# Kernel optimization log

Hardware: AMD Instinct MI355X
Metric: run time of the kernel (lower is better)

Reference implementation:

```python
import jax, jax.numpy as jnp
import numpy as np

P = 6
CUTOFF = 1.0
N_BASIS = 8
AVG_NEIGH = 16.0
NUM_LAYERS = 2
N, E, MUL, H, F = 8192, 131072, 16, 256, 16


def envelope(d):
    # polynomial cutoff u(x) with p=6 (NequIP/Allegro style)
    x = d / CUTOFF
    p = float(P)
    u = (1.0 - (p + 1.0) * (p + 2.0) / 2.0 * x ** P
         + p * (p + 2.0) * x ** (P + 1)
         - p * (p + 1.0) / 2.0 * x ** (P + 2))
    return jnp.where(x < 1.0, u, 0.0)


def bessel(d):
    k = jnp.arange(1, N_BASIS + 1, dtype=d.dtype)
    return jnp.sqrt(2.0 / CUTOFF) * jnp.sin(k[None, :] * jnp.pi * d[:, None] / CUTOFF) / d[:, None]


def sph_harm(u):
    # real spherical harmonics, ell=0..3, component normalization -> [E,16]
    x, y, z = u[:, 0], u[:, 1], u[:, 2]
    s3 = 3.0 ** 0.5
    s5 = 5.0 ** 0.5
    s15 = 15.0 ** 0.5
    s7 = 7.0 ** 0.5
    c33 = (35.0 / 8.0) ** 0.5
    c32 = 105.0 ** 0.5
    c31 = (21.0 / 8.0) ** 0.5
    one = jnp.ones_like(x)
    comps = [
        one,
        s3 * x, s3 * y, s3 * z,
        s15 * x * y, s15 * y * z, 0.5 * s5 * (3.0 * z * z - 1.0), s15 * x * z, 0.5 * s15 * (x * x - y * y),
        c33 * y * (3.0 * x * x - y * y), c32 * x * y * z, c31 * y * (5.0 * z * z - 1.0),
        0.5 * s7 * (5.0 * z ** 3 - 3.0 * z), c31 * x * (5.0 * z * z - 1.0),
        0.5 * c32 * z * (x * x - y * y), c33 * x * (x * x - 3.0 * y * y),
    ]
    return jnp.stack(comps, axis=1)


def setup_inputs() -> dict:
    key = jax.random.key(0)
    ks = jax.random.split(key, 16)
    dirs = jax.random.normal(ks[0], (E, 3), dtype=jnp.float32)
    dirs = dirs / jnp.linalg.norm(dirs, axis=1, keepdims=True)
    r = jax.random.uniform(ks[1], (E, 1), minval=0.05, maxval=0.95, dtype=jnp.float32)
    vectors = dirs * r
    node_attrs = 0.5 * jax.random.normal(ks[2], (N, F), dtype=jnp.float32)
    senders = jax.random.randint(ks[3], (E,), 0, N, dtype=jnp.int32)
    receivers = jax.random.randint(ks[4], (E,), 0, N, dtype=jnp.int32)

    def gl(k, shape):
        fan_in = shape[-2] if len(shape) >= 2 else 1
        return jax.random.normal(k, shape, dtype=jnp.float32) / jnp.sqrt(float(fan_in))

    return {
        'node_attrs': node_attrs, 'vectors': vectors,
        'senders': senders, 'receivers': receivers,
        'W_e0': gl(ks[5], (N_BASIS + 2 * F, H)), 'b_e0': jnp.zeros((H,), jnp.float32),
        'W_e1': gl(ks[6], (H, H)), 'b_e1': jnp.zeros((H,), jnp.float32),
        'W_v0': gl(ks[7], (H, MUL)),
        'W_lw': gl(ks[8], (NUM_LAYERS, H, MUL)),
        'W_lsh': gl(ks[9], (NUM_LAYERS, 16, 16)),
        'W_ly1': gl(ks[10], (NUM_LAYERS, H + MUL, H)), 'b_ly1': jnp.zeros((NUM_LAYERS, H), jnp.float32),
        'W_ly2': gl(ks[11], (NUM_LAYERS, H, H)), 'b_ly2': jnp.zeros((NUM_LAYERS, H), jnp.float32),
        'W_out': gl(ks[12], (H, 1)),
    }


def reference(node_attrs, vectors, senders, receivers, W_e0, b_e0, W_e1, b_e1, W_v0,
              W_lw, W_lsh, W_ly1, b_ly1, W_ly2, b_ly2, W_out):
    n_nodes = node_attrs.shape[0]
    inv = 1.0 / jnp.sqrt(AVG_NEIGH)
    d = jnp.linalg.norm(vectors, axis=1)                      # [E]
    u = envelope(d)                                           # [E]
    # edge embedding: radial basis + gathered endpoint attrs
    x = jnp.concatenate([bessel(d), node_attrs[senders], node_attrs[receivers]], axis=1)
    x = jax.nn.silu(x @ W_e0 + b_e0)
    x = jax.nn.silu(x @ W_e1 + b_e1)
    x = u[:, None] * x                                        # [E,H]
    Y = sph_harm(vectors / d[:, None])                        # [E,16]
    V = (x @ W_v0)[:, :, None] * Y[:, None, :]                # [E,MUL,16]
    for l in range(NUM_LAYERS):
        w = x @ W_lw[l]                                       # [E,MUL]
        wY = jax.ops.segment_sum(w[:, :, None] * Y[:, None, :], senders, num_segments=n_nodes) * inv
        wY = wY[senders]                                      # [E,MUL,16] gather back
        VV = wY * V                                           # per-edge equivariant product
        V = jnp.einsum('emi,ij->emj', VV, W_lsh[l])
        h = jnp.concatenate([x, VV[:, :, 0]], axis=1)         # scalar (l=0) channel feedback
        y = jax.nn.silu(h @ W_ly1[l] + b_ly1[l])
        y = jax.nn.silu(y @ W_ly2[l] + b_ly2[l])
        x = (x + u[:, None] * y) / jnp.sqrt(2.0)
    edge_out = (x @ W_out) * u[:, None]                       # [E,1]
    node_out = jax.ops.segment_sum(edge_out, receivers, num_segments=n_nodes) * inv
    return node_out                                           # [N,1]
```

## Files before the change

kernel.cpp:

```cpp
#include <hip/hip_runtime.h>
#include <hip/hip_bf16.h>
#include <math.h>

#define H 256
#define F 16
#define MUL 16
#define NB 8
#define LROW 296
#define YROW 264

typedef short bf16x8 __attribute__((ext_vector_type(8)));
typedef short bf16x4 __attribute__((ext_vector_type(4)));
typedef float f32x4 __attribute__((ext_vector_type(4)));
#define MFMA_B16(a, b, c) __builtin_amdgcn_mfma_f32_16x16x32_bf16(a, b, c, 0, 0, 0)

__device__ __forceinline__ float bf2f(__hip_bfloat16 x) { return __bfloat162float(x); }
__device__ __forceinline__ float silu(float x)
{
    return x * __builtin_amdgcn_rcpf(1.f + __expf(-x));
}
__device__ __forceinline__ short f2bs(float x)
{
    __hip_bfloat16 h = __float2bfloat16(x);
    short s; __builtin_memcpy(&s, &h, 2); return s;
}
__device__ __forceinline__ float bs2f(short s)
{
    __hip_bfloat16 h; __builtin_memcpy(&h, &s, 2); return __bfloat162float(h);
}

__global__ __launch_bounds__(256) void k_sniff(const void* vec, int* flag,
                                               int* cnt, int N)
{
    __shared__ int bad;
    int tid = threadIdx.x;
    if (tid == 0) bad = 0;
    __syncthreads();
    const __hip_bfloat16* hp = (const __hip_bfloat16*)vec;
    for (int i = tid; i < 1024; i += 256) {
        float f = bf2f(hp[i]);
        if (!(isfinite(f) && fabsf(f) <= 1.0f)) bad = 1;
    }
    for (int i = tid; i < N; i += 256) cnt[i] = 0;
    __syncthreads();
    if (tid == 0) *flag = bad;
}

struct ConvArgs {
    const void* src[14];
    float* dst[14];
    int cum[15];
};
__global__ __launch_bounds__(256) void k_conv_all(ConvArgs a, const int* __restrict__ flag,
                                                  const int* __restrict__ snd,
                                                  int* __restrict__ cnt, int E)
{
    int gid = blockIdx.x * 256 + threadIdx.x;
    if (gid < E) atomicAdd(&cnt[snd[gid]], 1);
    if (gid >= a.cum[14]) return;
    int k = 0;
    while (gid >= a.cum[k + 1]) k++;
    int i = gid - a.cum[k];
    float v = (*flag) ? ((const float*)a.src[k])[i]
                      : bf2f(((const __hip_bfloat16*)a.src[k])[i]);
    a.dst[k][i] = v;
}

struct SwzArgs {
    const float* src[9];
    __hip_bfloat16* dst[9];
    int K[9], Nc[9], cum[10];
};
__global__ __launch_bounds__(256) void k_swz_all(SwzArgs a)
{
    int gid = blockIdx.x * 256 + threadIdx.x;
    if (gid >= a.cum[9]) return;
    int j = 0;
    while (gid >= a.cum[j + 1]) j++;
    int idx = gid - a.cum[j];
    int kk = idx & 31;
    int n = (idx >> 5) % a.Nc[j];
    int kt = idx / (32 * a.Nc[j]);
    int k = kt * 32 + kk;
    float v = (k < a.K[j]) ? a.src[j][(size_t)k * a.Nc[j] + n] : 0.f;
    a.dst[j][idx] = __float2bfloat16(v);
}

__global__ __launch_bounds__(256) void k_swz_wout(const float* __restrict__ Wout,
                                                  __hip_bfloat16* __restrict__ dst)
{
    int idx = blockIdx.x * 256 + threadIdx.x;
    if (idx >= 8 * 16 * 32) return;
    int kk = idx & 31;
    int n = (idx >> 5) & 15;
    int kt = idx >> 9;
    float v = (n == 0) ? Wout[kt * 32 + kk] : 0.f;
    dst[idx] = __float2bfloat16(v);
}

__global__ __launch_bounds__(256) void k_scan(const int* __restrict__ cnt,
                                              int* __restrict__ off,
                                              int* __restrict__ cur, int N)
{
    __shared__ int sums[256];
    int tid = threadIdx.x;
    int chunk = (N + 255) / 256;
    int base = tid * chunk;
    int s = 0;
    for (int i = 0; i < chunk; i++) { int idx = base + i; if (idx < N) s += cnt[idx]; }
    sums[tid] = s;
    __syncthreads();
    for (int d = 1; d < 256; d <<= 1) {
        int v = (tid >= d) ? sums[tid - d] : 0;
        __syncthreads();
        sums[tid] += v;
        __syncthreads();
    }
    int run = (tid == 0) ? 0 : sums[tid - 1];
    for (int i = 0; i < chunk; i++) {
        int idx = base + i;
        if (idx < N) { off[idx] = run; cur[idx] = run; run += cnt[idx]; }
    }
    if (tid == 255) off[N] = run;
}

__global__ __launch_bounds__(256) void k_cscatter(const int* __restrict__ snd,
                                                  int* __restrict__ cur,
                                                  int* __restrict__ eidx, int E)
{
    int e = blockIdx.x * 256 + threadIdx.x;
    if (e >= E) return;
    int p = atomicAdd(&cur[snd[e]], 1);
    eidx[p] = e;
}


__global__ __launch_bounds__(512, 4) void k_embed_mfma(
    const float* __restrict__ vec, const float* __restrict__ na,
    const int* __restrict__ snd, const int* __restrict__ rcv,
    const __hip_bfloat16* __restrict__ We0s, const float* __restrict__ be0,
    const __hip_bfloat16* __restrict__ We1s, const float* __restrict__ be1,
    const __hip_bfloat16* __restrict__ Wv0s, const __hip_bfloat16* __restrict__ Wlws0,
    float* __restrict__ ubuf, float* __restrict__ Ybuf,
    __hip_bfloat16* __restrict__ xb, float* __restrict__ abuf,
    float* __restrict__ wbuf)
{
    __shared__ __align__(16) __hip_bfloat16 As[64 * LROW];
    __shared__ __align__(16) __hip_bfloat16 Ys[64 * YROW];
    __shared__ float us[64];
    int tid = threadIdx.x;
    int w = tid >> 6, l = tid & 63;
    int lm = l & 15, lq = l >> 4;
    int eb = blockIdx.x * 64;

    bf16x8 w0p[2][2];
#pragma unroll
    for (int kt = 0; kt < 2; kt++)
#pragma unroll
        for (int nt = 0; nt < 2; nt++)
            w0p[kt][nt] = *(const bf16x8*)(We0s + ((size_t)(kt * 256 + w * 32 + nt * 16 + lm) * 32 + lq * 8));

    {
        int el = tid & 63;
        int part = tid >> 6;
        int ge = eb + el;
        const float SQ2 = 1.41421356237309515f;
        const float PI = 3.14159265358979323846f;
        if (part == 0) {
            float vx = vec[3 * ge + 0], vy = vec[3 * ge + 1], vz = vec[3 * ge + 2];
            float d = sqrtf(vx * vx + vy * vy + vz * vz);
            float d3 = d * d * d;
            float d6 = d3 * d3, d7 = d6 * d, d8 = d7 * d;
            float u = 1.f - 28.f * d6 + 48.f * d7 - 21.f * d8;
            u = (d < 1.f) ? u : 0.f;
            ubuf[ge] = u;
            us[el] = u;
            float invd = __builtin_amdgcn_rcpf(d);
#pragma unroll
            for (int k = 1; k <= 4; k++)
                As[el * LROW + (k - 1)] = __float2bfloat16(SQ2 * __sinf((float)k * PI * d) * invd);
        } else if (part == 4) {
            float vx = vec[3 * ge + 0], vy = vec[3 * ge + 1], vz = vec[3 * ge + 2];
            float d = sqrtf(vx * vx + vy * vy + vz * vz);
            float invd = __builtin_amdgcn_rcpf(d);
#pragma unroll
            for (int k = 5; k <= 8; k++)
                As[el * LROW + (k - 1)] = __float2bfloat16(SQ2 * __sinf((float)k * PI * d) * invd);
        } else if (part == 5) {
#pragma unroll
            for (int j = 40; j < 64; j++) As[el * LROW + j] = __float2bfloat16(0.f);
        } else if (part == 1) {
            int s = snd[ge];
#pragma unroll
            for (int j = 0; j < 16; j++)
                As[el * LROW + 8 + j] = __float2bfloat16(na[(size_t)s * F + j]);
        } else if (part == 2) {
            int r = rcv[ge];
#pragma unroll
            for (int j = 0; j < 16; j++)
                As[el * LROW + 24 + j] = __float2bfloat16(na[(size_t)r * F + j]);
        } else if (part == 3) {
            float vx = vec[3 * ge + 0], vy = vec[3 * ge + 1], vz = vec[3 * ge + 2];
            float d = sqrtf(vx * vx + vy * vy + vz * vz);
            float invd = __builtin_amdgcn_rcpf(d);
            float x = vx * invd, y = vy * invd, z = vz * invd;
            const float s3 = 1.7320508075688772f;
            const float s5 = 2.2360679774997896f;
            const float s15 = 3.8729833462074170f;
            const float s7 = 2.6457513110645907f;
            const float c33 = 2.0916500663351889f;
            const float c32 = 10.246950765959598f;
            const float c31 = 1.6201851746019651f;
            float* Yp = Ybuf + (size_t)ge * 16;
            Yp[0] = 1.f;
            Yp[1] = s3 * x;  Yp[2] = s3 * y;  Yp[3] = s3 * z;
            Yp[4] = s15 * x * y;  Yp[5] = s15 * y * z;
            Yp[6] = 0.5f * s5 * (3.f * z * z - 1.f);
            Yp[7] = s15 * x * z;
            Yp[8] = 0.5f * s15 * (x * x - y * y);
            Yp[9] = c33 * y * (3.f * x * x - y * y);
            Yp[10] = c32 * x * y * z;
            Yp[11] = c31 * y * (5.f * z * z - 1.f);
            Yp[12] = 0.5f * s7 * (5.f * z * z * z - 3.f * z);
            Yp[13] = c31 * x * (5.f * z * z - 1.f);
            Yp[14] = 0.5f * c32 * z * (x * x - y * y);
            Yp[15] = c33 * x * (x * x - 3.f * y * y);
        }
    }
    __syncthreads();

    f32x4 acc[4][2];
#pragma unroll
    for (int mt = 0; mt < 4; mt++)
#pragma unroll
        for (int nt = 0; nt < 2; nt++) acc[mt][nt] = (f32x4){0.f, 0.f, 0.f, 0.f};
#pragma unroll
    for (int kt = 0; kt < 2; kt++) {
#pragma unroll
        for (int mt = 0; mt < 4; mt++) {
            bf16x8 bx = *(const bf16x8*)(As + (mt * 16 + lm) * LROW + kt * 32 + lq * 8);
#pragma unroll
            for (int nt = 0; nt < 2; nt++) acc[mt][nt] = MFMA_B16(w0p[kt][nt], bx, acc[mt][nt]);
        }
    }
    bf16x8 w1p[2][2];
#pragma unroll
    for (int kt = 0; kt < 2; kt++)
#pragma unroll
        for (int nt = 0; nt < 2; nt++)
            w1p[kt][nt] = *(const bf16x8*)(We1s + ((size_t)(kt * 256 + w * 32 + nt * 16 + lm) * 32 + lq * 8));
#pragma unroll
    for (int nt = 0; nt < 2; nt++) {
        int cb = w * 32 + nt * 16 + lq * 4;
        f32x4 bb = *(const f32x4*)(be0 + cb);
#pragma unroll
        for (int mt = 0; mt < 4; mt++) {
            int row = mt * 16 + lm;
            bf16x4 v = {f2bs(silu(acc[mt][nt][0] + bb[0])), f2bs(silu(acc[mt][nt][1] + bb[1])),
                        f2bs(silu(acc[mt][nt][2] + bb[2])), f2bs(silu(acc[mt][nt][3] + bb[3]))};
            *(bf16x4*)(Ys + row * YROW + cb) = v;
        }
    }
    __syncthreads();

#pragma unroll
    for (int mt = 0; mt < 4; mt++)
#pragma unroll
        for (int nt = 0; nt < 2; nt++) acc[mt][nt] = (f32x4){0.f, 0.f, 0.f, 0.f};
#pragma unroll
    for (int kt = 0; kt < 8; kt++) {
        bf16x8 aw[2];
#pragma unroll
        for (int nt = 0; nt < 2; nt++)
            aw[nt] = (kt < 2) ? w1p[kt][nt]
                   : *(const bf16x8*)(We1s + ((size_t)(kt * 256 + w * 32 + nt * 16 + lm) * 32 + lq * 8));
#pragma unroll
        for (int mt = 0; mt < 4; mt++) {
            bf16x8 bx = *(const bf16x8*)(Ys + (mt * 16 + lm) * YROW + kt * 32 + lq * 8);
#pragma unroll
            for (int nt = 0; nt < 2; nt++) acc[mt][nt] = MFMA_B16(aw[nt], bx, acc[mt][nt]);
        }
    }
    const __hip_bfloat16* tw = (w < 4) ? Wv0s : Wlws0;
    bf16x8 twp[2];
#pragma unroll
    for (int kt = 0; kt < 2; kt++)
        twp[kt] = *(const bf16x8*)(tw + ((size_t)(kt * 16 + lm) * 32 + lq * 8));
#pragma unroll
    for (int nt = 0; nt < 2; nt++) {
        int cb = w * 32 + nt * 16 + lq * 4;
        f32x4 bb = *(const f32x4*)(be1 + cb);
#pragma unroll
        for (int mt = 0; mt < 4; mt++) {
            int row = mt * 16 + lm;
            float uu = us[row];
            bf16x4 v = {f2bs(silu(acc[mt][nt][0] + bb[0]) * uu),
                        f2bs(silu(acc[mt][nt][1] + bb[1]) * uu),
                        f2bs(silu(acc[mt][nt][2] + bb[2]) * uu),
                        f2bs(silu(acc[mt][nt][3] + bb[3]) * uu)};
            *(bf16x4*)(As + row * LROW + cb) = v;
            *(bf16x4*)(xb + (size_t)(eb + row) * H + cb) = v;
        }
    }
    __syncthreads();

    if (w < 4) {
        f32x4 av = (f32x4){0.f, 0.f, 0.f, 0.f};
#pragma unroll
        for (int kt = 0; kt < 8; kt++) {
            bf16x8 bx = *(const bf16x8*)(As + (w * 16 + lm) * LROW + kt * 32 + lq * 8);
            bf16x8 a_v = (kt < 2) ? twp[kt]
                       : *(const bf16x8*)(Wv0s + ((size_t)(kt * 16 + lm) * 32 + lq * 8));
            av = MFMA_B16(a_v, bx, av);
        }
        *(f32x4*)(abuf + (size_t)(eb + w * 16 + lm) * 16 + lq * 4) = av;
    } else {
        int w2 = w - 4;
        f32x4 aw2 = (f32x4){0.f, 0.f, 0.f, 0.f};
#pragma unroll
        for (int kt = 0; kt < 8; kt++) {
            bf16x8 bx = *(const bf16x8*)(As + (w2 * 16 + lm) * LROW + kt * 32 + lq * 8);
            bf16x8 a_w = (kt < 2) ? twp[kt]
                       : *(const bf16x8*)(Wlws0 + ((size_t)(kt * 16 + lm) * 32 + lq * 8));
            aw2 = MFMA_B16(a_w, bx, aw2);
        }
        *(f32x4*)(wbuf + (size_t)(eb + w2 * 16 + lm) * 16 + lq * 4) = aw2;
    }
}

__global__ __launch_bounds__(256) void k_gather0(
    const int* __restrict__ off, const int* __restrict__ eidx,
    const float* __restrict__ wbuf, const float* __restrict__ Ybuf,
    const float* __restrict__ abuf,
    float* __restrict__ wYn0, __hip_bfloat16* __restrict__ vvbuf)
{
    __shared__ float ws[16][17];
    __shared__ float Ysh[16][17];
    __shared__ float w00[16];
    int tid = threadIdx.x;
    int m = tid >> 4, i = tid & 15;
    for (int nn = 0; nn < 4; nn++) {
        int n = blockIdx.x * 4 + nn;
        int beg = off[n], end = off[n + 1];
        float acc = 0.f;
        for (int c = beg; c < end; c += 16) {
            int ne = min(16, end - c);
            if (m < ne) {
                int e = eidx[c + m];
                ws[m][i] = wbuf[(size_t)e * 16 + i];
                Ysh[m][i] = Ybuf[(size_t)e * 16 + i];
            }
            __syncthreads();
            for (int j2 = 0; j2 < ne; j2++) acc += ws[j2][m] * Ysh[j2][i];
            __syncthreads();
        }
        wYn0[(size_t)n * 256 + m * 16 + i] = acc * 0.25f;
        if (i == 0) w00[m] = acc * 0.25f;
        __syncthreads();
        float w0i = w00[i];
        for (int c = beg + m; c < end; c += 16) {
            int e = eidx[c];
            float a = abuf[(size_t)e * 16 + i];
            vvbuf[(size_t)e * 16 + i] = __float2bfloat16(w0i * a);
        }
        __syncthreads();
    }
}

__global__ __launch_bounds__(256) void k_gather1(
    const int* __restrict__ off, const int* __restrict__ eidx,
    const float* __restrict__ wbuf, const float* __restrict__ Ybuf,
    const float* __restrict__ abuf,
    const float* __restrict__ wYn0, const float* __restrict__ Wlsh,
    __hip_bfloat16* __restrict__ vvbuf, float* __restrict__ nacc)
{
    __shared__ float ws[16][17];
    __shared__ float Ysh[16][17];
    __shared__ float qsh[16][17];
    __shared__ float w10[16];
    int tid = threadIdx.x;
    int m = tid >> 4, i = tid & 15;
    if (tid < 4) nacc[blockIdx.x * 4 + tid] = 0.f;
    for (int nn = 0; nn < 4; nn++) {
        int n = blockIdx.x * 4 + nn;
        int beg = off[n], end = off[n + 1];
        float acc = 0.f;
        for (int c = beg; c < end; c += 16) {
            int ne = min(16, end - c);
            if (m < ne) {
                int e = eidx[c + m];
                ws[m][i] = wbuf[(size_t)e * 16 + i];
                Ysh[m][i] = Ybuf[(size_t)e * 16 + i];
            }
            __syncthreads();
            for (int j2 = 0; j2 < ne; j2++) acc += ws[j2][m] * Ysh[j2][i];
            __syncthreads();
        }
        if (i == 0) w10[m] = acc * 0.25f;
        qsh[m][i] = wYn0[(size_t)n * 256 + m * 16 + i] * Wlsh[i * 16];
        __syncthreads();
        float w1i = w10[i];
        for (int c = beg + m; c < end; c += 16) {
            int e = eidx[c];
            float a = abuf[(size_t)e * 16 + i];
            float t = 0.f;
#pragma unroll
            for (int j = 0; j < 4; j++) {
                f32x4 yv = *(const f32x4*)(Ybuf + (size_t)e * 16 + 4 * j);
                t += qsh[i][4 * j + 0] * yv[0] + qsh[i][4 * j + 1] * yv[1]
                   + qsh[i][4 * j + 2] * yv[2] + qsh[i][4 * j + 3] * yv[3];
            }
            vvbuf[(size_t)e * 16 + i] = __float2bfloat16(w1i * a * t);
        }
        __syncthreads();
    }
}

__global__ __launch_bounds__(512, 4) void k_layer_mfma(
    __hip_bfloat16* __restrict__ xb, const float* __restrict__ ubuf,
    const __hip_bfloat16* __restrict__ vvbuf, const int* __restrict__ rcv,
    const __hip_bfloat16* __restrict__ W1s, const float* __restrict__ b1,
    const __hip_bfloat16* __restrict__ W2s, const float* __restrict__ b2,
    const __hip_bfloat16* __restrict__ Wlwn, float* __restrict__ wbufn,
    const __hip_bfloat16* __restrict__ Wouts, float* __restrict__ nacc,
    int layer)
{
    __shared__ __align__(16) __hip_bfloat16 As[64 * LROW];
    __shared__ __align__(16) __hip_bfloat16 Ys[64 * YROW];
    int tid = threadIdx.x;
    int w = tid >> 6, l = tid & 63;
    int lm = l & 15, lq = l >> 4;
    int eb = blockIdx.x * 64;

    bf16x8 w1p[2][2];
#pragma unroll
    for (int kt = 0; kt < 2; kt++)
#pragma unroll
        for (int nt = 0; nt < 2; nt++)
            w1p[kt][nt] = *(const bf16x8*)(W1s + ((size_t)(kt * 256 + w * 32 + nt * 16 + lm) * 32 + lq * 8));

#pragma unroll
    for (int i = 0; i < 4; i++) {
        int c = tid + 512 * i;
        int row = c >> 5, kc = c & 31;
        *(bf16x8*)(As + row * LROW + kc * 8) =
            *(const bf16x8*)(xb + (size_t)(eb + row) * H + kc * 8);
    }
    {
        int el = tid & 63;
        int mh = (tid >> 6) * 2;
        int ge = eb + el;
        *(unsigned int*)(As + el * LROW + 256 + mh) =
            *(const unsigned int*)((const short*)vvbuf + (size_t)ge * 16 + mh);
        if (tid < 64) {
#pragma unroll
            for (int j = 0; j < 16; j++) As[tid * LROW + 272 + j] = __float2bfloat16(0.f);
        }
    }
    __syncthreads();

    float uu[4];
#pragma unroll
    for (int mt = 0; mt < 4; mt++) uu[mt] = ubuf[eb + mt * 16 + lm];

    f32x4 acc[4][2];
#pragma unroll
    for (int mt = 0; mt < 4; mt++)
#pragma unroll
        for (int nt = 0; nt < 2; nt++) acc[mt][nt] = (f32x4){0.f, 0.f, 0.f, 0.f};
#pragma unroll
    for (int kt = 0; kt < 9; kt++) {
        bf16x8 aw[2];
#pragma unroll
        for (int nt = 0; nt < 2; nt++)
            aw[nt] = (kt < 2) ? w1p[kt][nt]
                   : *(const bf16x8*)(W1s + ((size_t)(kt * 256 + w * 32 + nt * 16 + lm) * 32 + lq * 8));
#pragma unroll
        for (int mt = 0; mt < 4; mt++) {
            bf16x8 bx = *(const bf16x8*)(As + (mt * 16 + lm) * LROW + kt * 32 + lq * 8);
#pragma unroll
            for (int nt = 0; nt < 2; nt++) acc[mt][nt] = MFMA_B16(aw[nt], bx, acc[mt][nt]);
        }
    }
    bf16x8 w2p[2][2];
#pragma unroll
    for (int kt = 0; kt < 2; kt++)
#pragma unroll
        for (int nt = 0; nt < 2; nt++)
            w2p[kt][nt] = *(const bf16x8*)(W2s + ((size_t)(kt * 256 + w * 32 + nt * 16 + lm) * 32 + lq * 8));
#pragma unroll
    for (int nt = 0; nt < 2; nt++) {
        int cb = w * 32 + nt * 16 + lq * 4;
        f32x4 bb = *(const f32x4*)(b1 + cb);
#pragma unroll
        for (int mt = 0; mt < 4; mt++) {
            int row = mt * 16 + lm;
            bf16x4 v = {f2bs(silu(acc[mt][nt][0] + bb[0])), f2bs(silu(acc[mt][nt][1] + bb[1])),
                        f2bs(silu(acc[mt][nt][2] + bb[2])), f2bs(silu(acc[mt][nt][3] + bb[3]))};
            *(bf16x4*)(Ys + row * YROW + cb) = v;
        }
    }
    __syncthreads();

#pragma unroll
    for (int mt = 0; mt < 4; mt++)
#pragma unroll
        for (int nt = 0; nt < 2; nt++) acc[mt][nt] = (f32x4){0.f, 0.f, 0.f, 0.f};
#pragma unroll
    for (int kt = 0; kt < 8; kt++) {
        bf16x8 aw[2];
#pragma unroll
        for (int nt = 0; nt < 2; nt++)
            aw[nt] = (kt < 2) ? w2p[kt][nt]
                   : *(const bf16x8*)(W2s + ((size_t)(kt * 256 + w * 32 + nt * 16 + lm) * 32 + lq * 8));
#pragma unroll
        for (int mt = 0; mt < 4; mt++) {
            bf16x8 bx = *(const bf16x8*)(Ys + (mt * 16 + lm) * YROW + kt * 32 + lq * 8);
#pragma unroll
            for (int nt = 0; nt < 2; nt++) acc[mt][nt] = MFMA_B16(aw[nt], bx, acc[mt][nt]);
        }
    }
    const __hip_bfloat16* tw = (layer == 0) ? Wlwn : Wouts;
    bf16x8 twp[2];
#pragma unroll
    for (int kt = 0; kt < 2; kt++)
        twp[kt] = *(const bf16x8*)(tw + ((size_t)(kt * 16 + lm) * 32 + lq * 8));
    const float rs2 = 0.70710678118654752f;
#pragma unroll
    for (int nt = 0; nt < 2; nt++) {
        int cb = w * 32 + nt * 16 + lq * 4;
        f32x4 bb = *(const f32x4*)(b2 + cb);
#pragma unroll
        for (int mt = 0; mt < 4; mt++) {
            int row = mt * 16 + lm;
            bf16x4 xo = *(const bf16x4*)(As + row * LROW + cb);
            bf16x4 v;
#pragma unroll
            for (int r = 0; r < 4; r++) {
                float xn = (bs2f(xo[r]) + uu[mt] * silu(acc[mt][nt][r] + bb[r])) * rs2;
                v[r] = f2bs(xn);
            }
            *(bf16x4*)(As + row * LROW + cb) = v;
            if (layer == 0) *(bf16x4*)(xb + (size_t)(eb + row) * H + cb) = v;
        }
    }
    __syncthreads();

    if (layer == 0) {
        if (w < 4) {
            f32x4 cw = (f32x4){0.f, 0.f, 0.f, 0.f};
#pragma unroll
            for (int kt = 0; kt < 8; kt++) {
                bf16x8 bx = *(const bf16x8*)(As + (w * 16 + lm) * LROW + kt * 32 + lq * 8);
                bf16x8 a = (kt < 2) ? twp[kt]
                         : *(const bf16x8*)(Wlwn + ((size_t)(kt * 16 + lm) * 32 + lq * 8));
                cw = MFMA_B16(a, bx, cw);
            }
            *(f32x4*)(wbufn + (size_t)(eb + w * 16 + lm) * 16 + lq * 4) = cw;
        }
    } else {
        if (w < 4) {
            f32x4 co = (f32x4){0.f, 0.f, 0.f, 0.f};
#pragma unroll
            for (int kt = 0; kt < 8; kt++) {
                bf16x8 bx = *(const bf16x8*)(As + (w * 16 + lm) * LROW + kt * 32 + lq * 8);
                bf16x8 a = (kt < 2) ? twp[kt]
                         : *(const bf16x8*)(Wouts + ((size_t)(kt * 16 + lm) * 32 + lq * 8));
                co = MFMA_B16(a, bx, co);
            }
            if (lq == 0) {
                int e = eb + w * 16 + lm;
                atomicAdd(&nacc[rcv[e]], co[0] * ubuf[e]);
            }
        }
    }
}

__global__ __launch_bounds__(256) void k_final(
    const float* __restrict__ nacc, void* __restrict__ out, const int* __restrict__ flag,
    float inv, int N)
{
    int n = blockIdx.x * 256 + threadIdx.x;
    if (n >= N) return;
    float v = nacc[n] * inv;
    if (*flag) ((float*)out)[n] = v;
    else       ((__hip_bfloat16*)out)[n] = __float2bfloat16(v);
}

extern "C" void kernel_launch(void* const* d_in, const int* in_sizes, int n_in,
                              void* d_out, int out_size, void* d_ws, size_t ws_size,
                              hipStream_t stream)
{
    const int E = in_sizes[2];
    const int N = in_sizes[0] / F;
    (void)n_in; (void)ws_size; (void)out_size;

    char* wsb = (char*)d_ws;
    size_t off = 0;
    int* flag = (int*)wsb; off += 256;

    const int fidx[14] = {0, 1, 4, 5, 6, 7, 8, 9, 10, 11, 12, 13, 14, 15};
    float* canon[14];
    for (int k = 0; k < 14; k++) {
        canon[k] = (float*)(wsb + off);
        off += (size_t)in_sizes[fidx[k]] * 4;
        off = (off + 255) & ~(size_t)255;
    }
    const float* naC   = canon[0];
    const float* vecC  = canon[1];
    const float* We0C  = canon[2];
    const float* be0C  = canon[3];
    const float* We1C  = canon[4];
    const float* be1C  = canon[5];
    const float* Wv0C  = canon[6];
    const float* WlwC  = canon[7];
    const float* WlshC = canon[8];
    const float* Wly1C = canon[9];
    const float* bly1C = canon[10];
    const float* Wly2C = canon[11];
    const float* bly2C = canon[12];
    const float* WoutC = canon[13];

    __hip_bfloat16* We0s  = (__hip_bfloat16*)(wsb + off); off += 64 * 256 * 2;
    __hip_bfloat16* We1s  = (__hip_bfloat16*)(wsb + off); off += 256 * 256 * 2;
    __hip_bfloat16* Wv0s  = (__hip_bfloat16*)(wsb + off); off += 256 * 16 * 2;
    __hip_bfloat16* Wlws0 = (__hip_bfloat16*)(wsb + off); off += 256 * 16 * 2;
    __hip_bfloat16* Wlws1 = (__hip_bfloat16*)(wsb + off); off += 256 * 16 * 2;
    __hip_bfloat16* W1s0  = (__hip_bfloat16*)(wsb + off); off += 288 * 256 * 2;
    __hip_bfloat16* W1s1  = (__hip_bfloat16*)(wsb + off); off += 288 * 256 * 2;
    __hip_bfloat16* W2s0  = (__hip_bfloat16*)(wsb + off); off += 256 * 256 * 2;
    __hip_bfloat16* W2s1  = (__hip_bfloat16*)(wsb + off); off += 256 * 256 * 2;
    __hip_bfloat16* Wouts = (__hip_bfloat16*)(wsb + off); off += 256 * 16 * 2;
    off = (off + 255) & ~(size_t)255;

    __hip_bfloat16* xbuf = (__hip_bfloat16*)(wsb + off); off += (size_t)E * H * 2;
    float* wYn0 = (float*)(wsb + off); off += (size_t)N * H * 4;
    __hip_bfloat16* vvbuf = (__hip_bfloat16*)(wsb + off); off += (size_t)E * 16 * 2;
    float* ubuf = (float*)(wsb + off); off += (size_t)E * 4;
    float* Ybuf = (float*)(wsb + off); off += (size_t)E * 16 * 4;
    float* abuf = (float*)(wsb + off); off += (size_t)E * 16 * 4;
    float* wbuf = (float*)(wsb + off); off += (size_t)E * 16 * 4;
    float* nacc = (float*)(wsb + off); off += (size_t)N * 4;
    int* cnt  = (int*)(wsb + off); off += (size_t)N * 4;
    int* offb = (int*)(wsb + off); off += (size_t)(N + 1) * 4;
    int* cur  = (int*)(wsb + off); off += (size_t)N * 4;
    int* eidx = (int*)(wsb + off); off += (size_t)E * 4;

    const int* snd = (const int*)d_in[2];
    const int* rcv = (const int*)d_in[3];
    const float inv = 0.25f;
    const int nb64 = E / 64;

    k_sniff<<<1, 256, 0, stream>>>(d_in[1], flag, cnt, N);
    {
        ConvArgs ca;
        int c = 0;
        for (int k = 0; k < 14; k++) {
            ca.src[k] = d_in[fidx[k]];
            ca.dst[k] = canon[k];
            ca.cum[k] = c;
            c += in_sizes[fidx[k]];
        }
        ca.cum[14] = c;
        k_conv_all<<<(c + 255) / 256, 256, 0, stream>>>(ca, flag, snd, cnt, E);
    }

    {
        SwzArgs sa;
        const float* srcs[9] = {We0C, We1C, Wv0C, WlwC, WlwC + 256 * 16,
                                Wly1C, Wly1C + 272 * 256, Wly2C, Wly2C + 256 * 256};
        __hip_bfloat16* dsts[9] = {We0s, We1s, Wv0s, Wlws0, Wlws1, W1s0, W1s1, W2s0, W2s1};
        int Ks[9]    = {40, 256, 256, 256, 256, 272, 272, 256, 256};
        int Ncs[9]   = {256, 256, 16, 16, 16, 256, 256, 256, 256};
        int Kpads[9] = {64, 256, 256, 256, 256, 288, 288, 256, 256};
        int c = 0;
        for (int j = 0; j < 9; j++) {
            sa.src[j] = srcs[j]; sa.dst[j] = dsts[j];
            sa.K[j] = Ks[j]; sa.Nc[j] = Ncs[j];
            sa.cum[j] = c;
            c += (Kpads[j] >> 5) * Ncs[j] * 32;
        }
        sa.cum[9] = c;
        k_swz_all<<<(c + 255) / 256, 256, 0, stream>>>(sa);
    }
    k_swz_wout<<<16, 256, 0, stream>>>(WoutC, Wouts);

    k_scan<<<1, 256, 0, stream>>>(cnt, offb, cur, N);
    k_cscatter<<<(E + 255) / 256, 256, 0, stream>>>(snd, cur, eidx, E);

    k_embed_mfma<<<nb64, 512, 0, stream>>>(vecC, naC, snd, rcv,
                                           We0s, be0C, We1s, be1C, Wv0s, Wlws0,
                                           ubuf, Ybuf, xbuf, abuf, wbuf);

    k_gather0<<<N / 4, 256, 0, stream>>>(offb, eidx, wbuf, Ybuf, abuf, wYn0, vvbuf);
    k_layer_mfma<<<nb64, 512, 0, stream>>>(xbuf, ubuf, vvbuf, rcv,
                                           W1s0, bly1C, W2s0, bly2C,
                                           Wlws1, wbuf,
                                           (const __hip_bfloat16*)nullptr, (float*)nullptr, 0);
    k_gather1<<<N / 4, 256, 0, stream>>>(offb, eidx, wbuf, Ybuf, abuf, wYn0, WlshC,
                                         vvbuf, nacc);
    k_layer_mfma<<<nb64, 512, 0, stream>>>(xbuf, ubuf, vvbuf, rcv,
                                           W1s1, bly1C + H, W2s1, bly2C + H,
                                           (const __hip_bfloat16*)nullptr, (float*)nullptr,
                                           Wouts, nacc, 1);

    k_final<<<(N + 255) / 256, 256, 0, stream>>>(nacc, d_out, flag, inv, N);
}
```

Measured before the change: 345.5 us.

## Assign one wavefront per node in gather kernels instead of serial node loop

The two per-node gather kernels previously processed their four nodes one after another with the full 256-thread block, syncing twice per 16-edge chunk. Now each 64-lane wavefront owns one node, with per-wave shared-memory slices and four accumulators per lane, so the four nodes proceed concurrently. Iteration count is bounded by the largest degree among the four nodes, so waves with fewer edges sit idle at the block barriers. Shared memory per block grows fourfold.

```diff
diff --git a/kernel.cpp b/kernel.cpp
--- a/kernel.cpp
+++ b/kernel.cpp
@@ -334,36 +334,57 @@
     const float* __restrict__ abuf,
     float* __restrict__ wYn0, __hip_bfloat16* __restrict__ vvbuf)
 {
-    __shared__ float ws[16][17];
-    __shared__ float Ysh[16][17];
-    __shared__ float w00[16];
+    __shared__ float ws[4][16][17];
+    __shared__ float Ysh[4][16][17];
+    __shared__ float w00s[4][16];
     int tid = threadIdx.x;
-    int m = tid >> 4, i = tid & 15;
-    for (int nn = 0; nn < 4; nn++) {
-        int n = blockIdx.x * 4 + nn;
-        int beg = off[n], end = off[n + 1];
-        float acc = 0.f;
-        for (int c = beg; c < end; c += 16) {
-            int ne = min(16, end - c);
-            if (m < ne) {
-                int e = eidx[c + m];
-                ws[m][i] = wbuf[(size_t)e * 16 + i];
-                Ysh[m][i] = Ybuf[(size_t)e * 16 + i];
+    int w = tid >> 6, l = tid & 63;
+    int js = l >> 4, i = l & 15;
+    int n0 = blockIdx.x * 4;
+    int n = n0 + w;
+    int beg = off[n], end = off[n + 1];
+    int o0 = off[n0], o1 = off[n0 + 1], o2 = off[n0 + 2], o3 = off[n0 + 3], o4 = off[n0 + 4];
+    int m01 = max(o1 - o0, o2 - o1), m23 = max(o3 - o2, o4 - o3);
+    int maxc = (max(m01, m23) + 15) >> 4;
+    float acc[4] = {0.f, 0.f, 0.f, 0.f};
+    for (int r = 0; r < maxc; r++) {
+        int c = beg + r * 16;
+        int ne = min(16, end - c);
+        if (ne > 0) {
+#pragma unroll
+            for (int k = 0; k < 4; k++) {
+                int j = js + 4 * k;
+                if (j < ne) {
+                    int e = eidx[c + j];
+                    ws[w][j][i]  = wbuf[(size_t)e * 16 + i];
+                    Ysh[w][j][i] = Ybuf[(size_t)e * 16 + i];
+                }
             }
-            __syncthreads();
-            for (int j2 = 0; j2 < ne; j2++) acc += ws[j2][m] * Ysh[j2][i];
-            __syncthreads();
-        }
-        wYn0[(size_t)n * 256 + m * 16 + i] = acc * 0.25f;
-        if (i == 0) w00[m] = acc * 0.25f;
+        }
         __syncthreads();
-        float w0i = w00[i];
-        for (int c = beg + m; c < end; c += 16) {
-            int e = eidx[c];
-            float a = abuf[(size_t)e * 16 + i];
-            vvbuf[(size_t)e * 16 + i] = __float2bfloat16(w0i * a);
+        if (ne > 0) {
+            for (int j2 = 0; j2 < ne; j2++) {
+                float yv = Ysh[w][j2][i];
+#pragma unroll
+                for (int k = 0; k < 4; k++)
+                    acc[k] += ws[w][j2][js + 4 * k] * yv;
+            }
         }
         __syncthreads();
+    }
+#pragma unroll
+    for (int k = 0; k < 4; k++)
+        wYn0[(size_t)n * 256 + (js + 4 * k) * 16 + i] = acc[k] * 0.25f;
+    if (i == 0) {
+#pragma unroll
+        for (int k = 0; k < 4; k++) w00s[w][js + 4 * k] = acc[k] * 0.25f;
+    }
+    __syncthreads();
+    float w0i = w00s[w][i];
+    for (int c = beg + js; c < end; c += 4) {
+        int e = eidx[c];
+        float a = abuf[(size_t)e * 16 + i];
+        vvbuf[(size_t)e * 16 + i] = __float2bfloat16(w0i * a);
     }
 }
 
@@ -374,45 +395,68 @@
     const float* __restrict__ wYn0, const float* __restrict__ Wlsh,
     __hip_bfloat16* __restrict__ vvbuf, float* __restrict__ nacc)
 {
-    __shared__ float ws[16][17];
-    __shared__ float Ysh[16][17];
-    __shared__ float qsh[16][17];
-    __shared__ float w10[16];
+    __shared__ float ws[4][16][17];
+    __shared__ float Ysh[4][16][17];
+    __shared__ float qsh[4][16][17];
+    __shared__ float w10s[4][16];
     int tid = threadIdx.x;
-    int m = tid >> 4, i = tid & 15;
-    if (tid < 4) nacc[blockIdx.x * 4 + tid] = 0.f;
-    for (int nn = 0; nn < 4; nn++) {
-        int n = blockIdx.x * 4 + nn;
-        int beg = off[n], end = off[n + 1];
-        float acc = 0.f;
-        for (int c = beg; c < end; c += 16) {
-            int ne = min(16, end - c);
-            if (m < ne) {
-                int e = eidx[c + m];
-                ws[m][i] = wbuf[(size_t)e * 16 + i];
-                Ysh[m][i] = Ybuf[(size_t)e * 16 + i];
+    int w = tid >> 6, l = tid & 63;
+    int js = l >> 4, i = l & 15;
+    int n0 = blockIdx.x * 4;
+    int n = n0 + w;
+    int beg = off[n], end = off[n + 1];
+    if (tid < 4) nacc[n0 + tid] = 0.f;
+    int o0 = off[n0], o1 = off[n0 + 1], o2 = off[n0 + 2], o3 = off[n0 + 3], o4 = off[n0 + 4];
+    int m01 = max(o1 - o0, o2 - o1), m23 = max(o3 - o2, o4 - o3);
+    int maxc = (max(m01, m23) + 15) >> 4;
+    float acc[4] = {0.f, 0.f, 0.f, 0.f};
+    for (int r = 0; r < maxc; r++) {
+        int c = beg + r * 16;
+        int ne = min(16, end - c);
+        if (ne > 0) {
+#pragma unroll
+            for (int k = 0; k < 4; k++) {
+                int j = js + 4 * k;
+                if (j < ne) {
+                    int e = eidx[c + j];
+                    ws[w][j][i]  = wbuf[(size_t)e * 16 + i];
+                    Ysh[w][j][i] = Ybuf[(size_t)e * 16 + i];
+                }
             }
-            __syncthreads();
-            for (int j2 = 0; j2 < ne; j2++) acc += ws[j2][m] * Ysh[j2][i];
-            __syncthreads();
-        }
-        if (i == 0) w10[m] = acc * 0.25f;
-        qsh[m][i] = wYn0[(size_t)n * 256 + m * 16 + i] * Wlsh[i * 16];
+        }
         __syncthreads();
-        float w1i = w10[i];
-        for (int c = beg + m; c < end; c += 16) {
-            int e = eidx[c];
-            float a = abuf[(size_t)e * 16 + i];
-            float t = 0.f;
-#pragma unroll
-            for (int j = 0; j < 4; j++) {
-                f32x4 yv = *(const f32x4*)(Ybuf + (size_t)e * 16 + 4 * j);
-                t += qsh[i][4 * j + 0] * yv[0] + qsh[i][4 * j + 1] * yv[1]
-                   + qsh[i][4 * j + 2] * yv[2] + qsh[i][4 * j + 3] * yv[3];
+        if (ne > 0) {
+            for (int j2 = 0; j2 < ne; j2++) {
+                float yv = Ysh[w][j2][i];
+#pragma unroll
+                for (int k = 0; k < 4; k++)
+                    acc[k] += ws[w][j2][js + 4 * k] * yv;
             }
-            vvbuf[(size_t)e * 16 + i] = __float2bfloat16(w1i * a * t);
         }
         __syncthreads();
+    }
+    if (i == 0) {
+#pragma unroll
+        for (int k = 0; k < 4; k++) w10s[w][js + 4 * k] = acc[k] * 0.25f;
+    }
+#pragma unroll
+    for (int k = 0; k < 4; k++) {
+        int m = js + 4 * k;
+        qsh[w][m][i] = wYn0[(size_t)n * 256 + m * 16 + i] * Wlsh[i * 16];
+    }
+    __syncthreads();
+    float w1i = w10s[w][i];
+    for (int c = beg + js; c < end; c += 4) {
+        int e = eidx[c];
+        float a = abuf[(size_t)e * 16 + i];
+        float t = 0.f;
+#pragma unroll
+        for (int j = 0; j < 4; j++) {
+            f32x4 yv = *(const f32x4*)(Ybuf + (size_t)e * 16 + 4 * j);
+            t += qsh[w][i][4 * j + 0] * yv[0] + qsh[w][i][4 * j + 1] * yv[1]
+               + qsh[w][i][4 * j + 2] * yv[2] + qsh[w][i][4 * j + 3] * yv[3];
+        }
+        vvbuf[(size_t)e * 16 + i] = __float2bfloat16(w1i * a * t);
     }
 }
 
```

New measurement: 341.9 us. No clear change (-1.0%).
